# Performance work log

Hardware: AMD Instinct MI355X
Metric: run time of the kernel (lower is better)

## Reference

```python
import jax, jax.numpy as jnp
import numpy as np

HID = 64   # hid_dim // 2 inside pocket_att_net2
H = 8      # n_heads


def _dist_mask(d):
    """get_mask: 8 distance bands, each carrying 1/d inside its band, else 0.
    band i (i=0..6): i < d <= i+3 ; band 7: d > 7.  Output [B, 8, Nl, Np]."""
    safe = jnp.where(d > 0, d, 1.0)
    inv = jnp.where(d > 0, 1.0 / safe, 0.0)
    bands = []
    for i in range(8):
        if i < 7:
            m = (d > float(i)) & (d <= float(i + 3))
        else:
            m = d > 7.0
        bands.append(jnp.where(m, inv, 0.0))
    return jnp.stack(bands, axis=1)


def setup_inputs() -> dict:
    key = jax.random.key(0)
    ks = jax.random.split(key, 20)
    B, Nl, Np = 16, 256, 2048
    s = 0.05
    inp = {
        "ligand": jax.random.normal(ks[0], (B, Nl, HID), jnp.float32),
        "prot":   jax.random.normal(ks[1], (B, Np, HID), jnp.float32),
        "dist":   jax.random.uniform(ks[2], (B, Nl, Np), jnp.float32) * 10.0,
        # projection weights (jax convention: x @ W + b)
        "w_l1": jax.random.normal(ks[3], (HID, HID * H), jnp.float32) * s,
        "b_l1": jnp.zeros((HID * H,), jnp.float32),
        "w_l2": jax.random.normal(ks[4], (HID, HID * H), jnp.float32) * s,
        "b_l2": jnp.zeros((HID * H,), jnp.float32),
        "w_p1": jax.random.normal(ks[5], (HID, HID * H), jnp.float32) * s,
        "b_p1": jnp.zeros((HID * H,), jnp.float32),
        "w_p2": jax.random.normal(ks[6], (HID, HID * H), jnp.float32) * s,
        "b_p2": jnp.zeros((HID * H,), jnp.float32),
        "fc11_w": jax.random.normal(ks[7], (HID * H, HID), jnp.float32) * s,
        "fc11_b": jnp.zeros((HID,), jnp.float32),
        "fc12_w": jax.random.normal(ks[8], (2 * HID, HID), jnp.float32) * s,
        "fc12_b": jnp.zeros((HID,), jnp.float32),
        "fc21_w": jax.random.normal(ks[9], (HID * H, HID), jnp.float32) * s,
        "fc21_b": jnp.zeros((HID,), jnp.float32),
        "fc22_w": jax.random.normal(ks[10], (2 * HID, HID), jnp.float32) * s,
        "fc22_b": jnp.zeros((HID,), jnp.float32),
    }
    return inp


def _proj(x, w, b):
    B, N, _ = x.shape
    h = jax.nn.relu(x @ w + b)                      # [B, N, H*HID]
    return h.reshape(B, N, H, HID).transpose(0, 2, 1, 3)  # [B, H, N, HID]


def reference(ligand, prot, dist, w_l1, b_l1, w_l2, b_l2, w_p1, b_p1, w_p2, b_p2,
              fc11_w, fc11_b, fc12_w, fc12_b, fc21_w, fc21_b, fc22_w, fc22_b):
    B, Nl, _ = ligand.shape
    Np = prot.shape[1]
    inter = _dist_mask(dist)                        # [B, H, Nl, Np]

    l1 = _proj(ligand, w_l1, b_l1)
    l2 = _proj(ligand, w_l2, b_l2)
    p1 = _proj(prot, w_p1, b_p1)
    p2 = _proj(prot, w_p2, b_p2)

    scale = jnp.sqrt(jnp.float32(HID))
    energy = jnp.einsum('bhld,bhpd->bhlp', l1, p1) / scale
    att = jax.nn.softmax(energy * inter, axis=-1)   # dropout = identity (eval)

    l3 = jnp.einsum('bhlp,bhpd->bhld', att, p2)
    l3 = l3.transpose(0, 2, 1, 3).reshape(B, Nl, H * HID)
    l3 = jnp.concatenate([l3 @ fc11_w + fc11_b, ligand], axis=2)
    l3 = jax.nn.relu(l3 @ fc12_w + fc12_b)          # [B, Nl, HID]

    p3 = jnp.einsum('bhlp,bhld->bhpd', att, l2)
    p3 = p3.transpose(0, 2, 1, 3).reshape(B, Np, H * HID)
    p3 = jnp.concatenate([p3 @ fc21_w + fc21_b, prot], axis=2)
    p3 = jax.nn.relu(p3 @ fc22_w + fc22_b)          # [B, Np, HID]

    return jnp.concatenate([l3, p3], axis=1)        # [B, Nl+Np, HID]
```

## Files before the change

kernel.cpp:

```cpp
#include <hip/hip_runtime.h>
#include <hip/hip_bf16.h>

typedef _Float16 f16x8 __attribute__((ext_vector_type(8)));
typedef _Float16 f16x4 __attribute__((ext_vector_type(4)));
typedef float f32x4 __attribute__((ext_vector_type(4)));

#define B_   16
#define NL   256
#define NP   2048
#define NH   8

static __device__ __forceinline__ f32x4 mfma16(f16x8 a, f16x8 b, f32x4 c) {
  return __builtin_amdgcn_mfma_f32_16x16x32_f16(a, b, c, 0, 0, 0);
}

__global__ __launch_bounds__(256) void proj_kernel(
    const float* __restrict__ x, const float* __restrict__ W, const float* __restrict__ bias,
    _Float16* __restrict__ outA, _Float16* __restrict__ outB, int N, int mode)
{
  __shared__ float xt[64][68];
  const int t = threadIdx.x;
  const int n0 = blockIdx.x * 64;
  const int h  = blockIdx.y;
  const int b  = blockIdx.z;

  const float* xp = x + ((size_t)b * N + n0) * 64;
#pragma unroll
  for (int i = 0; i < 4; ++i) {
    int flat = (i * 256 + t) * 4;
    f32x4 v = *(const f32x4*)(xp + flat);
    *(f32x4*)&xt[flat >> 6][flat & 63] = v;
  }
  __syncthreads();

  const int nb = (t >> 4) * 4;
  const int db = (t & 15) * 4;

  float acc[4][4];
#pragma unroll
  for (int i = 0; i < 4; ++i)
#pragma unroll
    for (int j = 0; j < 4; ++j) acc[i][j] = bias[h * 64 + db + j];

  const float* wp = W + h * 64 + db;
#pragma unroll 8
  for (int k = 0; k < 64; ++k) {
    f32x4 wq = *(const f32x4*)(wp + (size_t)k * 512);
    float a0 = xt[nb + 0][k], a1 = xt[nb + 1][k], a2 = xt[nb + 2][k], a3 = xt[nb + 3][k];
#pragma unroll
    for (int j = 0; j < 4; ++j) {
      acc[0][j] += a0 * wq[j];
      acc[1][j] += a1 * wq[j];
      acc[2][j] += a2 * wq[j];
      acc[3][j] += a3 * wq[j];
    }
  }

  if (mode == 0) {
#pragma unroll
    for (int i = 0; i < 4; ++i) {
      f16x4 hv, lv;
#pragma unroll
      for (int j = 0; j < 4; ++j) {
        float v = fmaxf(acc[i][j], 0.f);
        _Float16 hi = (_Float16)v;
        hv[j] = hi;
        lv[j] = (_Float16)((v - (float)hi) * 2048.0f);
      }
      size_t idx = (((size_t)b * NH + h) * N + n0 + nb + i) * 64 + db;
      *(f16x4*)(outA + idx) = hv;
      *(f16x4*)(outB + idx) = lv;
    }
  } else {
#pragma unroll
    for (int j = 0; j < 4; ++j) {
      f16x4 tv;
#pragma unroll
      for (int i = 0; i < 4; ++i) tv[i] = (_Float16)fmaxf(acc[i][j], 0.f);
      size_t idx = (((size_t)b * NH + h) * 64 + db + j) * N + n0 + nb;
      *(f16x4*)(outA + idx) = tv;
    }
  }
}

__global__ __launch_bounds__(64) void flash_l3_kernel(
    const _Float16* __restrict__ l1h, const _Float16* __restrict__ l1l,
    const _Float16* __restrict__ p1h, const _Float16* __restrict__ p1l,
    const _Float16* __restrict__ p2t, const float* __restrict__ dist,
    float* __restrict__ l3c, float* __restrict__ mrow, float* __restrict__ rsrow)
{
  const int wid = blockIdx.x;
  const int lt = wid & 15;
  const int bh = wid >> 4;
  const int b = bh >> 3, h = bh & 7;
  const int lane = threadIdx.x;
  const int g = lane >> 4, c = lane & 15;
  const int l0 = lt * 16;

  __shared__ _Float16 P[16][72];

  const size_t l1off = ((size_t)bh * NL + l0 + c) * 64;
  f16x8 aLh[2], aLl[2];
  aLh[0] = *(const f16x8*)(l1h + l1off + g * 8);
  aLh[1] = *(const f16x8*)(l1h + l1off + 32 + g * 8);
  aLl[0] = *(const f16x8*)(l1l + l1off + g * 8);
  aLl[1] = *(const f16x8*)(l1l + l1off + 32 + g * 8);

  f32x4 accO[4];
#pragma unroll
  for (int dt = 0; dt < 4; ++dt) accO[dt] = (f32x4){0.f, 0.f, 0.f, 0.f};
  float m_r[4] = {-INFINITY, -INFINITY, -INFINITY, -INFINITY};
  float s_r[4] = {0.f, 0.f, 0.f, 0.f};

  const float* dbase = dist + ((size_t)b * NL + l0) * NP;
  const _Float16* p1hb = p1h + (size_t)bh * NP * 64;
  const _Float16* p1lb = p1l + (size_t)bh * NP * 64;
  const _Float16* p2tb = p2t + (size_t)bh * 64 * NP;
  const float fh = (float)h;

  for (int P0 = 0; P0 < NP; P0 += 64) {
    float mev[4][4];
    float cmax[4] = {-INFINITY, -INFINITY, -INFINITY, -INFINITY};
#pragma unroll
    for (int s = 0; s < 4; ++s) {
      const int p = P0 + s * 16 + c;
      const _Float16* ph = p1hb + (size_t)p * 64;
      const _Float16* pl = p1lb + (size_t)p * 64;
      f16x8 bh0 = *(const f16x8*)(ph + g * 8);
      f16x8 bh1 = *(const f16x8*)(ph + 32 + g * 8);
      f16x8 bl0 = *(const f16x8*)(pl + g * 8);
      f16x8 bl1 = *(const f16x8*)(pl + 32 + g * 8);
      f32x4 e  = (f32x4){0.f, 0.f, 0.f, 0.f};
      f32x4 ec = (f32x4){0.f, 0.f, 0.f, 0.f};
      e  = mfma16(aLh[0], bh0, e);  e  = mfma16(aLh[1], bh1, e);
      ec = mfma16(aLh[0], bl0, ec); ec = mfma16(aLh[1], bl1, ec);
      ec = mfma16(aLl[0], bh0, ec); ec = mfma16(aLl[1], bh1, ec);
#pragma unroll
      for (int r = 0; r < 4; ++r) {
        float dv = dbase[(size_t)(g * 4 + r) * NP + p];
        float ev = (e[r] + ec[r] * (1.0f / 2048.0f)) * 0.125f;
        bool cond = (h < 7) ? (dv > fh && dv <= fh + 3.0f) : (dv > 7.0f);
        float m = cond ? ev / dv : 0.0f;
        mev[s][r] = m;
        cmax[r] = fmaxf(cmax[r], m);
      }
    }
#pragma unroll
    for (int mask = 1; mask < 16; mask <<= 1)
#pragma unroll
      for (int r = 0; r < 4; ++r)
        cmax[r] = fmaxf(cmax[r], __shfl_xor(cmax[r], mask, 64));

#pragma unroll
    for (int r = 0; r < 4; ++r) {
      float mn  = fmaxf(m_r[r], cmax[r]);
      float fac = __expf(m_r[r] - mn);
      m_r[r] = mn;
      float ss = 0.f;
#pragma unroll
      for (int s = 0; s < 4; ++s) {
        float pv = __expf(mev[s][r] - mn);
        ss += pv;
        P[g * 4 + r][s * 16 + c] = (_Float16)pv;
      }
      s_r[r] = s_r[r] * fac + ss;
#pragma unroll
      for (int dt = 0; dt < 4; ++dt) accO[dt][r] *= fac;
    }
    __syncthreads();
#pragma unroll
    for (int kk = 0; kk < 2; ++kk) {
      f16x8 aP = *(const f16x8*)&P[c][kk * 32 + g * 8];
#pragma unroll
      for (int dt = 0; dt < 4; ++dt) {
        f16x8 bV = *(const f16x8*)(p2tb + (size_t)(dt * 16 + c) * NP + P0 + kk * 32 + g * 8);
        accO[dt] = mfma16(aP, bV, accO[dt]);
      }
    }
    __syncthreads();
  }

#pragma unroll
  for (int mask = 1; mask < 16; mask <<= 1)
#pragma unroll
    for (int r = 0; r < 4; ++r) s_r[r] += __shfl_xor(s_r[r], mask, 64);

#pragma unroll
  for (int r = 0; r < 4; ++r) {
    float inv = 1.0f / s_r[r];
#pragma unroll
    for (int dt = 0; dt < 4; ++dt) accO[dt][r] *= inv;
  }
#pragma unroll
  for (int dt = 0; dt < 4; ++dt)
#pragma unroll
    for (int r = 0; r < 4; ++r)
      l3c[((size_t)b * NL + l0 + g * 4 + r) * 512 + h * 64 + dt * 16 + c] = accO[dt][r];

  if (c == 0) {
#pragma unroll
    for (int r = 0; r < 4; ++r) {
      size_t li = (size_t)bh * NL + l0 + g * 4 + r;
      mrow[li]  = m_r[r];
      rsrow[li] = 1.0f / s_r[r];
    }
  }
}

__global__ __launch_bounds__(64) void p3_kernel(
    const _Float16* __restrict__ p1h, const _Float16* __restrict__ p1l,
    const _Float16* __restrict__ l1h, const _Float16* __restrict__ l1l,
    const _Float16* __restrict__ l2t, const float* __restrict__ dist,
    const float* __restrict__ mrow, const float* __restrict__ rsrow,
    float* __restrict__ p3c)
{
  const int wid = blockIdx.x;
  const int pt = wid & 127;
  const int bh = wid >> 7;
  const int b = bh >> 3, h = bh & 7;
  const int lane = threadIdx.x;
  const int g = lane >> 4, c = lane & 15;
  const int p0 = pt * 16;

  __shared__ _Float16 PT[16][40];

  const size_t poff = ((size_t)bh * NP + p0 + c) * 64;
  f16x8 aPh[2], aPl[2];
  aPh[0] = *(const f16x8*)(p1h + poff + g * 8);
  aPh[1] = *(const f16x8*)(p1h + poff + 32 + g * 8);
  aPl[0] = *(const f16x8*)(p1l + poff + g * 8);
  aPl[1] = *(const f16x8*)(p1l + poff + 32 + g * 8);

  f32x4 acc[4];
#pragma unroll
  for (int dt = 0; dt < 4; ++dt) acc[dt] = (f32x4){0.f, 0.f, 0.f, 0.f};

  const float* db_ = dist + (size_t)b * NL * NP;
  const _Float16* l1hb = l1h + (size_t)bh * NL * 64;
  const _Float16* l1lb = l1l + (size_t)bh * NL * 64;
  const _Float16* l2tb = l2t + (size_t)bh * 64 * NL;
  const float* mb = mrow + (size_t)bh * NL;
  const float* rb = rsrow + (size_t)bh * NL;
  const float fh = (float)h;

  for (int lc = 0; lc < NL; lc += 32) {
#pragma unroll
    for (int s = 0; s < 2; ++s) {
      const int l = lc + s * 16 + c;
      const _Float16* lhp = l1hb + (size_t)l * 64;
      const _Float16* llp = l1lb + (size_t)l * 64;
      f16x8 bh0 = *(const f16x8*)(lhp + g * 8);
      f16x8 bh1 = *(const f16x8*)(lhp + 32 + g * 8);
      f16x8 bl0 = *(const f16x8*)(llp + g * 8);
      f16x8 bl1 = *(const f16x8*)(llp + 32 + g * 8);
      f32x4 e  = (f32x4){0.f, 0.f, 0.f, 0.f};
      f32x4 ec = (f32x4){0.f, 0.f, 0.f, 0.f};
      e  = mfma16(aPh[0], bh0, e);  e  = mfma16(aPh[1], bh1, e);
      ec = mfma16(aPh[0], bl0, ec); ec = mfma16(aPh[1], bl1, ec);
      ec = mfma16(aPl[0], bh0, ec); ec = mfma16(aPl[1], bh1, ec);
      float ml = mb[l], rl = rb[l];
      f32x4 dq = *(const f32x4*)(db_ + (size_t)l * NP + p0 + g * 4);
#pragma unroll
      for (int r = 0; r < 4; ++r) {
        float ev = (e[r] + ec[r] * (1.0f / 2048.0f)) * 0.125f;
        float dv = dq[r];
        bool cond = (h < 7) ? (dv > fh && dv <= fh + 3.0f) : (dv > 7.0f);
        float m = cond ? ev / dv : 0.0f;
        float att = __expf(m - ml) * rl;
        PT[g * 4 + r][s * 16 + c] = (_Float16)att;
      }
    }
    __syncthreads();
    {
      f16x8 aA = *(const f16x8*)&PT[c][g * 8];
#pragma unroll
      for (int dt = 0; dt < 4; ++dt) {
        f16x8 bV = *(const f16x8*)(l2tb + (size_t)(dt * 16 + c) * NL + lc + g * 8);
        acc[dt] = mfma16(aA, bV, acc[dt]);
      }
    }
    __syncthreads();
  }

#pragma unroll
  for (int dt = 0; dt < 4; ++dt)
#pragma unroll
    for (int r = 0; r < 4; ++r)
      p3c[((size_t)b * NP + p0 + g * 4 + r) * 512 + h * 64 + dt * 16 + c] = acc[dt][r];
}

__global__ __launch_bounds__(256) void fc_out_kernel(
    const float* __restrict__ x3c, const float* __restrict__ xbase,
    const float* __restrict__ wA, const float* __restrict__ bA,
    const float* __restrict__ wB, const float* __restrict__ bB,
    float* __restrict__ out, int N, int out_off)
{
  __shared__ float xl[16][520];
  __shared__ float t1[16][68];
  __shared__ float xb[16][68];
  const int t = threadIdx.x;
  const int row0 = blockIdx.x * 16;

  const float* xp = x3c + (size_t)row0 * 512;
#pragma unroll
  for (int i = 0; i < 8; ++i) {
    int flat = (i * 256 + t) * 4;
    f32x4 v = *(const f32x4*)(xp + flat);
    *(f32x4*)&xl[flat >> 9][flat & 511] = v;
  }
  {
    const float* bp = xbase + (size_t)row0 * 64;
    int flat = t * 4;
    f32x4 v = *(const f32x4*)(bp + flat);
    *(f32x4*)&xb[flat >> 6][flat & 63] = v;
  }
  __syncthreads();

  const int r  = t >> 4;
  const int c4 = (t & 15) * 4;

  float acc[4];
#pragma unroll
  for (int j = 0; j < 4; ++j) acc[j] = bA[c4 + j];
  for (int k4 = 0; k4 < 128; ++k4) {
    f32x4 xq = *(const f32x4*)&xl[r][k4 * 4];
#pragma unroll
    for (int kk = 0; kk < 4; ++kk) {
      f32x4 wq = *(const f32x4*)(wA + (size_t)(k4 * 4 + kk) * 64 + c4);
#pragma unroll
      for (int j = 0; j < 4; ++j) acc[j] += xq[kk] * wq[j];
    }
  }
#pragma unroll
  for (int j = 0; j < 4; ++j) t1[r][c4 + j] = acc[j];
  __syncthreads();

  float a2[4];
#pragma unroll
  for (int j = 0; j < 4; ++j) a2[j] = bB[c4 + j];
  for (int k4 = 0; k4 < 32; ++k4) {
    f32x4 xq = (k4 < 16) ? *(const f32x4*)&t1[r][k4 * 4]
                         : *(const f32x4*)&xb[r][k4 * 4 - 64];
#pragma unroll
    for (int kk = 0; kk < 4; ++kk) {
      f32x4 wq = *(const f32x4*)(wB + (size_t)(k4 * 4 + kk) * 64 + c4);
#pragma unroll
      for (int j = 0; j < 4; ++j) a2[j] += xq[kk] * wq[j];
    }
  }
  const int row = row0 + r;
  const int b = row / N, n = row % N;
  f32x4 o;
#pragma unroll
  for (int j = 0; j < 4; ++j) o[j] = fmaxf(a2[j], 0.f);
  *(f32x4*)(out + (((size_t)b * (NL + NP)) + out_off + n) * 64 + c4) = o;
}

extern "C" void kernel_launch(void* const* d_in, const int* in_sizes, int n_in,
                              void* d_out, int out_size, void* d_ws, size_t ws_size,
                              hipStream_t stream)
{
  const float* ligand = (const float*)d_in[0];
  const float* prot   = (const float*)d_in[1];
  const float* dist   = (const float*)d_in[2];
  const float* w_l1   = (const float*)d_in[3];
  const float* b_l1   = (const float*)d_in[4];
  const float* w_l2   = (const float*)d_in[5];
  const float* b_l2   = (const float*)d_in[6];
  const float* w_p1   = (const float*)d_in[7];
  const float* b_p1   = (const float*)d_in[8];
  const float* w_p2   = (const float*)d_in[9];
  const float* b_p2   = (const float*)d_in[10];
  const float* fc11_w = (const float*)d_in[11];
  const float* fc11_b = (const float*)d_in[12];
  const float* fc12_w = (const float*)d_in[13];
  const float* fc12_b = (const float*)d_in[14];
  const float* fc21_w = (const float*)d_in[15];
  const float* fc21_b = (const float*)d_in[16];
  const float* fc22_w = (const float*)d_in[17];
  const float* fc22_b = (const float*)d_in[18];
  float* out = (float*)d_out;

  char* ws = (char*)d_ws;
  size_t off = 0;
  auto alloc = [&](size_t bytes) -> void* {
    void* p = ws + off;
    off += (bytes + 255) & ~(size_t)255;
    return p;
  };
  const size_t L1E = (size_t)B_ * NH * NL * 64;
  const size_t P1E = (size_t)B_ * NH * NP * 64;
  _Float16* l1h = (_Float16*)alloc(L1E * 2);
  _Float16* l1l = (_Float16*)alloc(L1E * 2);
  _Float16* p1h = (_Float16*)alloc(P1E * 2);
  _Float16* p1l = (_Float16*)alloc(P1E * 2);
  _Float16* l2t = (_Float16*)alloc(L1E * 2);
  _Float16* p2t = (_Float16*)alloc(P1E * 2);
  float* mrow  = (float*)alloc((size_t)B_ * NH * NL * 4);
  float* rsrow = (float*)alloc((size_t)B_ * NH * NL * 4);
  float* l3c = (float*)alloc((size_t)B_ * NL * 512 * 4);
  float* p3c = (float*)alloc((size_t)B_ * NP * 512 * 4);

  proj_kernel<<<dim3(NL / 64, NH, B_), 256, 0, stream>>>(ligand, w_l1, b_l1, l1h, l1l, NL, 0);
  proj_kernel<<<dim3(NL / 64, NH, B_), 256, 0, stream>>>(ligand, w_l2, b_l2, l2t, nullptr, NL, 1);
  proj_kernel<<<dim3(NP / 64, NH, B_), 256, 0, stream>>>(prot, w_p1, b_p1, p1h, p1l, NP, 0);
  proj_kernel<<<dim3(NP / 64, NH, B_), 256, 0, stream>>>(prot, w_p2, b_p2, p2t, nullptr, NP, 1);

  flash_l3_kernel<<<B_ * NH * (NL / 16), 64, 0, stream>>>(l1h, l1l, p1h, p1l, p2t, dist,
                                                          l3c, mrow, rsrow);
  p3_kernel<<<B_ * NH * (NP / 16), 64, 0, stream>>>(p1h, p1l, l1h, l1l, l2t, dist,
                                                    mrow, rsrow, p3c);

  fc_out_kernel<<<(B_ * NL) / 16, 256, 0, stream>>>(l3c, ligand, fc11_w, fc11_b,
                                                    fc12_w, fc12_b, out, NL, 0);
  fc_out_kernel<<<(B_ * NP) / 16, 256, 0, stream>>>(p3c, prot, fc21_w, fc21_b,
                                                    fc22_w, fc22_b, out, NP, NL);
}
```

Before: 880.7 us.

## Share dist tiles across heads via LDS and split-K the flash l3 pass

Both attention kernels now launch one 512-thread block per (tile, batch), with the 8 heads as 8 waves. Each block stages the dist tile once in shared memory, so dist is read from global memory once per batch instead of once per head. The l3 flash kernel also splits the protein axis into 4 chunks and writes partial max, sum and output to scratch that reuses the p3c buffer, and a new merge kernel combines them. Division is replaced by a fast reciprocal. The split adds an extra kernel launch and a round trip through partial buffers, and the approximate reciprocal may change results slightly.

Result: faster. 799.5 us (-9.2%).

```diff
diff --git a/kernel.cpp b/kernel.cpp
--- a/kernel.cpp
+++ b/kernel.cpp
@@ -9,6 +9,8 @@
 #define NL   256
 #define NP   2048
 #define NH   8
+#define PSPLIT 4
+#define PCHUNK (NP / PSPLIT)
 
 static __device__ __forceinline__ f32x4 mfma16(f16x8 a, f16x8 b, f32x4 c) {
   return __builtin_amdgcn_mfma_f32_16x16x32_f16(a, b, c, 0, 0, 0);
@@ -83,21 +85,24 @@
   }
 }
 
-__global__ __launch_bounds__(64) void flash_l3_kernel(
+__global__ __launch_bounds__(512) void flash_l3_kernel(
     const _Float16* __restrict__ l1h, const _Float16* __restrict__ l1l,
     const _Float16* __restrict__ p1h, const _Float16* __restrict__ p1l,
     const _Float16* __restrict__ p2t, const float* __restrict__ dist,
-    float* __restrict__ l3c, float* __restrict__ mrow, float* __restrict__ rsrow)
-{
-  const int wid = blockIdx.x;
-  const int lt = wid & 15;
-  const int bh = wid >> 4;
-  const int b = bh >> 3, h = bh & 7;
-  const int lane = threadIdx.x;
+    float* __restrict__ l3p, float* __restrict__ mpart, float* __restrict__ spart)
+{
+  const int lt = blockIdx.x;
+  const int sp = blockIdx.y;
+  const int b  = blockIdx.z;
+  const int t  = threadIdx.x;
+  const int h    = t >> 6;
+  const int lane = t & 63;
   const int g = lane >> 4, c = lane & 15;
   const int l0 = lt * 16;
-
-  __shared__ _Float16 P[16][72];
+  const int bh = b * NH + h;
+
+  __shared__ float distT[64][20];
+  __shared__ _Float16 P[NH][16][72];
 
   const size_t l1off = ((size_t)bh * NL + l0 + c) * 64;
   f16x8 aLh[2], aLl[2];
@@ -112,20 +117,29 @@
   float m_r[4] = {-INFINITY, -INFINITY, -INFINITY, -INFINITY};
   float s_r[4] = {0.f, 0.f, 0.f, 0.f};
 
-  const float* dbase = dist + ((size_t)b * NL + l0) * NP;
-  const _Float16* p1hb = p1h + (size_t)bh * NP * 64;
-  const _Float16* p1lb = p1l + (size_t)bh * NP * 64;
-  const _Float16* p2tb = p2t + (size_t)bh * 64 * NP;
-  const float fh = (float)h;
-
-  for (int P0 = 0; P0 < NP; P0 += 64) {
+  const float* dbase = dist + ((size_t)b * NL + l0) * NP + sp * PCHUNK;
+  const _Float16* p1hb = p1h + ((size_t)bh * NP + sp * PCHUNK) * 64;
+  const _Float16* p1lb = p1l + ((size_t)bh * NP + sp * PCHUNK) * 64;
+  const _Float16* p2tb = p2t + (size_t)bh * 64 * NP + sp * PCHUNK;
+  const float fh = (float)h, fh3 = fh + 3.0f;
+
+  const int dl_p = t & 63;
+  const int dl_l = t >> 6;
+
+  for (int P0 = 0; P0 < PCHUNK; P0 += 64) {
+    float dv0 = dbase[(size_t)dl_l * NP + P0 + dl_p];
+    float dv1 = dbase[(size_t)(dl_l + 8) * NP + P0 + dl_p];
+    __syncthreads();
+    distT[dl_p][dl_l]     = dv0;
+    distT[dl_p][dl_l + 8] = dv1;
+    __syncthreads();
+
     float mev[4][4];
     float cmax[4] = {-INFINITY, -INFINITY, -INFINITY, -INFINITY};
 #pragma unroll
     for (int s = 0; s < 4; ++s) {
-      const int p = P0 + s * 16 + c;
-      const _Float16* ph = p1hb + (size_t)p * 64;
-      const _Float16* pl = p1lb + (size_t)p * 64;
+      const _Float16* ph = p1hb + (size_t)(P0 + s * 16 + c) * 64;
+      const _Float16* pl = p1lb + (size_t)(P0 + s * 16 + c) * 64;
       f16x8 bh0 = *(const f16x8*)(ph + g * 8);
       f16x8 bh1 = *(const f16x8*)(ph + 32 + g * 8);
       f16x8 bl0 = *(const f16x8*)(pl + g * 8);
@@ -135,12 +149,13 @@
       e  = mfma16(aLh[0], bh0, e);  e  = mfma16(aLh[1], bh1, e);
       ec = mfma16(aLh[0], bl0, ec); ec = mfma16(aLh[1], bl1, ec);
       ec = mfma16(aLl[0], bh0, ec); ec = mfma16(aLl[1], bh1, ec);
+      f32x4 dq = *(const f32x4*)&distT[s * 16 + c][g * 4];
 #pragma unroll
       for (int r = 0; r < 4; ++r) {
-        float dv = dbase[(size_t)(g * 4 + r) * NP + p];
+        float dv = dq[r];
         float ev = (e[r] + ec[r] * (1.0f / 2048.0f)) * 0.125f;
-        bool cond = (h < 7) ? (dv > fh && dv <= fh + 3.0f) : (dv > 7.0f);
-        float m = cond ? ev / dv : 0.0f;
+        bool cond = (h < 7) ? (dv > fh && dv <= fh3) : (dv > 7.0f);
+        float m = cond ? ev * __builtin_amdgcn_rcpf(dv) : 0.0f;
         mev[s][r] = m;
         cmax[r] = fmaxf(cmax[r], m);
       }
@@ -161,7 +176,7 @@
       for (int s = 0; s < 4; ++s) {
         float pv = __expf(mev[s][r] - mn);
         ss += pv;
-        P[g * 4 + r][s * 16 + c] = (_Float16)pv;
+        P[h][g * 4 + r][s * 16 + c] = (_Float16)pv;
       }
       s_r[r] = s_r[r] * fac + ss;
 #pragma unroll
@@ -170,14 +185,13 @@
     __syncthreads();
 #pragma unroll
     for (int kk = 0; kk < 2; ++kk) {
-      f16x8 aP = *(const f16x8*)&P[c][kk * 32 + g * 8];
+      f16x8 aP = *(const f16x8*)&P[h][c][kk * 32 + g * 8];
 #pragma unroll
       for (int dt = 0; dt < 4; ++dt) {
         f16x8 bV = *(const f16x8*)(p2tb + (size_t)(dt * 16 + c) * NP + P0 + kk * 32 + g * 8);
         accO[dt] = mfma16(aP, bV, accO[dt]);
       }
     }
-    __syncthreads();
   }
 
 #pragma unroll
@@ -185,44 +199,73 @@
 #pragma unroll
     for (int r = 0; r < 4; ++r) s_r[r] += __shfl_xor(s_r[r], mask, 64);
 
-#pragma unroll
-  for (int r = 0; r < 4; ++r) {
-    float inv = 1.0f / s_r[r];
-#pragma unroll
-    for (int dt = 0; dt < 4; ++dt) accO[dt][r] *= inv;
-  }
+  float* lp = l3p + (size_t)sp * B_ * NL * 512;
 #pragma unroll
   for (int dt = 0; dt < 4; ++dt)
 #pragma unroll
     for (int r = 0; r < 4; ++r)
-      l3c[((size_t)b * NL + l0 + g * 4 + r) * 512 + h * 64 + dt * 16 + c] = accO[dt][r];
+      lp[((size_t)b * NL + l0 + g * 4 + r) * 512 + h * 64 + dt * 16 + c] = accO[dt][r];
 
   if (c == 0) {
 #pragma unroll
     for (int r = 0; r < 4; ++r) {
-      size_t li = (size_t)bh * NL + l0 + g * 4 + r;
-      mrow[li]  = m_r[r];
-      rsrow[li] = 1.0f / s_r[r];
-    }
-  }
-}
-
-__global__ __launch_bounds__(64) void p3_kernel(
+      size_t li = (size_t)sp * B_ * NH * NL + (size_t)bh * NL + l0 + g * 4 + r;
+      mpart[li] = m_r[r];
+      spart[li] = s_r[r];
+    }
+  }
+}
+
+__global__ __launch_bounds__(256) void merge_l3_kernel(
+    const float* __restrict__ l3p, const float* __restrict__ mpart, const float* __restrict__ spart,
+    float* __restrict__ l3c, float* __restrict__ mrow, float* __restrict__ rsrow)
+{
+  const int row = blockIdx.x * 4 + (threadIdx.x >> 6);
+  const int d   = threadIdx.x & 63;
+  const int l   = row & (NL - 1);
+  const int bh  = row >> 8;
+  const int b = bh >> 3, h = bh & 7;
+  const size_t srow = (size_t)B_ * NH * NL;
+
+  float mi[PSPLIT], si[PSPLIT];
+  float M = -INFINITY;
+#pragma unroll
+  for (int i = 0; i < PSPLIT; ++i) {
+    mi[i] = mpart[(size_t)i * srow + row];
+    si[i] = spart[(size_t)i * srow + row];
+    M = fmaxf(M, mi[i]);
+  }
+  const float* lp = l3p + ((size_t)b * NL + l) * 512 + h * 64 + d;
+  float S = 0.f, o = 0.f;
+#pragma unroll
+  for (int i = 0; i < PSPLIT; ++i) {
+    float w = __expf(mi[i] - M);
+    S += si[i] * w;
+    o += lp[(size_t)i * B_ * NL * 512] * w;
+  }
+  float rs = 1.0f / S;
+  l3c[((size_t)b * NL + l) * 512 + h * 64 + d] = o * rs;
+  if (d == 0) { mrow[row] = M; rsrow[row] = rs; }
+}
+
+__global__ __launch_bounds__(512) void p3_kernel(
     const _Float16* __restrict__ p1h, const _Float16* __restrict__ p1l,
     const _Float16* __restrict__ l1h, const _Float16* __restrict__ l1l,
     const _Float16* __restrict__ l2t, const float* __restrict__ dist,
     const float* __restrict__ mrow, const float* __restrict__ rsrow,
     float* __restrict__ p3c)
 {
-  const int wid = blockIdx.x;
-  const int pt = wid & 127;
-  const int bh = wid >> 7;
-  const int b = bh >> 3, h = bh & 7;
-  const int lane = threadIdx.x;
+  const int pt = blockIdx.x;
+  const int b  = blockIdx.y;
+  const int t  = threadIdx.x;
+  const int h    = t >> 6;
+  const int lane = t & 63;
   const int g = lane >> 4, c = lane & 15;
   const int p0 = pt * 16;
-
-  __shared__ _Float16 PT[16][40];
+  const int bh = b * NH + h;
+
+  __shared__ float distT[32][20];
+  __shared__ _Float16 PT[NH][16][40];
 
   const size_t poff = ((size_t)bh * NP + p0 + c) * 64;
   f16x8 aPh[2], aPl[2];
@@ -235,15 +278,23 @@
 #pragma unroll
   for (int dt = 0; dt < 4; ++dt) acc[dt] = (f32x4){0.f, 0.f, 0.f, 0.f};
 
-  const float* db_ = dist + (size_t)b * NL * NP;
+  const float* db_ = dist + (size_t)b * NL * NP + p0;
   const _Float16* l1hb = l1h + (size_t)bh * NL * 64;
   const _Float16* l1lb = l1l + (size_t)bh * NL * 64;
   const _Float16* l2tb = l2t + (size_t)bh * 64 * NL;
   const float* mb = mrow + (size_t)bh * NL;
   const float* rb = rsrow + (size_t)bh * NL;
-  const float fh = (float)h;
+  const float fh = (float)h, fh3 = fh + 3.0f;
+
+  const int dl_l = t >> 4;
+  const int dl_p = t & 15;
 
   for (int lc = 0; lc < NL; lc += 32) {
+    float dv = db_[(size_t)(lc + dl_l) * NP + dl_p];
+    __syncthreads();
+    distT[dl_l][dl_p] = dv;
+    __syncthreads();
+
 #pragma unroll
     for (int s = 0; s < 2; ++s) {
       const int l = lc + s * 16 + c;
@@ -259,27 +310,26 @@
       ec = mfma16(aPh[0], bl0, ec); ec = mfma16(aPh[1], bl1, ec);
       ec = mfma16(aPl[0], bh0, ec); ec = mfma16(aPl[1], bh1, ec);
       float ml = mb[l], rl = rb[l];
-      f32x4 dq = *(const f32x4*)(db_ + (size_t)l * NP + p0 + g * 4);
+      f32x4 dq = *(const f32x4*)&distT[s * 16 + c][g * 4];
 #pragma unroll
       for (int r = 0; r < 4; ++r) {
         float ev = (e[r] + ec[r] * (1.0f / 2048.0f)) * 0.125f;
-        float dv = dq[r];
-        bool cond = (h < 7) ? (dv > fh && dv <= fh + 3.0f) : (dv > 7.0f);
-        float m = cond ? ev / dv : 0.0f;
+        float dvv = dq[r];
+        bool cond = (h < 7) ? (dvv > fh && dvv <= fh3) : (dvv > 7.0f);
+        float m = cond ? ev * __builtin_amdgcn_rcpf(dvv) : 0.0f;
         float att = __expf(m - ml) * rl;
-        PT[g * 4 + r][s * 16 + c] = (_Float16)att;
+        PT[h][g * 4 + r][s * 16 + c] = (_Float16)att;
       }
     }
     __syncthreads();
     {
-      f16x8 aA = *(const f16x8*)&PT[c][g * 8];
+      f16x8 aA = *(const f16x8*)&PT[h][c][g * 8];
 #pragma unroll
       for (int dt = 0; dt < 4; ++dt) {
         f16x8 bV = *(const f16x8*)(l2tb + (size_t)(dt * 16 + c) * NL + lc + g * 8);
         acc[dt] = mfma16(aA, bV, acc[dt]);
       }
     }
-    __syncthreads();
   }
 
 #pragma unroll
@@ -398,18 +448,22 @@
   _Float16* p2t = (_Float16*)alloc(P1E * 2);
   float* mrow  = (float*)alloc((size_t)B_ * NH * NL * 4);
   float* rsrow = (float*)alloc((size_t)B_ * NH * NL * 4);
+  float* mpart = (float*)alloc((size_t)PSPLIT * B_ * NH * NL * 4);
+  float* spart = (float*)alloc((size_t)PSPLIT * B_ * NH * NL * 4);
   float* l3c = (float*)alloc((size_t)B_ * NL * 512 * 4);
   float* p3c = (float*)alloc((size_t)B_ * NP * 512 * 4);
+  float* l3p = p3c;
 
   proj_kernel<<<dim3(NL / 64, NH, B_), 256, 0, stream>>>(ligand, w_l1, b_l1, l1h, l1l, NL, 0);
   proj_kernel<<<dim3(NL / 64, NH, B_), 256, 0, stream>>>(ligand, w_l2, b_l2, l2t, nullptr, NL, 1);
   proj_kernel<<<dim3(NP / 64, NH, B_), 256, 0, stream>>>(prot, w_p1, b_p1, p1h, p1l, NP, 0);
   proj_kernel<<<dim3(NP / 64, NH, B_), 256, 0, stream>>>(prot, w_p2, b_p2, p2t, nullptr, NP, 1);
 
-  flash_l3_kernel<<<B_ * NH * (NL / 16), 64, 0, stream>>>(l1h, l1l, p1h, p1l, p2t, dist,
-                                                          l3c, mrow, rsrow);
-  p3_kernel<<<B_ * NH * (NP / 16), 64, 0, stream>>>(p1h, p1l, l1h, l1l, l2t, dist,
-                                                    mrow, rsrow, p3c);
+  flash_l3_kernel<<<dim3(NL / 16, PSPLIT, B_), 512, 0, stream>>>(
+      l1h, l1l, p1h, p1l, p2t, dist, l3p, mpart, spart);
+  merge_l3_kernel<<<(B_ * NH * NL) / 4, 256, 0, stream>>>(l3p, mpart, spart, l3c, mrow, rsrow);
+  p3_kernel<<<dim3(NP / 16, B_), 512, 0, stream>>>(p1h, p1l, l1h, l1l, l2t, dist,
+                                                   mrow, rsrow, p3c);
 
   fc_out_kernel<<<(B_ * NL) / 16, 256, 0, stream>>>(l3c, ligand, fc11_w, fc11_b,
                                                     fc12_w, fc12_b, out, NL, 0);
```
